# Kernel tuning notes

Measured on AMD Instinct MI355X. Metric: run time of the kernel, lower is better.

Reference implementation:

```python
import jax, jax.numpy as jnp
import numpy as np

B, N, D = 1, 128, 64
H, DH = 8, 64            # heads, per-head dim; dim_inner = dim*dim_head = 512
DI = H * DH              # 512
L = 2                    # max_degree
S = 1 + 2 * L            # 5 degree slots: (h, r_1..L, x_1..L)
MLP = 1024               # int(2.0 * dim_inner)
EPS = 1e-5


def _ln(x, g):
    m = x.mean(-1, keepdims=True)
    v = ((x - m) ** 2).mean(-1, keepdims=True)
    return (x - m) * jax.lax.rsqrt(v + EPS) * g


def setup_inputs() -> dict:
    key = jax.random.key(0)
    ks = jax.random.split(key, 16)
    rn = lambda k, s, sc=1.0: jax.random.normal(k, s, dtype=jnp.float32) * sc
    return {
        "h": rn(ks[0], (B, N, D)),
        "t_ij": rn(ks[1], (B, N, N, D)),
        "r1": rn(ks[2], (B, N, N, 3)),
        "r2": rn(ks[3], (B, N, N, 5)),
        "x1": rn(ks[4], (B, N, D, 3)),
        "x2": rn(ks[5], (B, N, D, 5)),
        "g_hi": jnp.ones((D,), jnp.float32),
        "g_hj": jnp.ones((D,), jnp.float32),
        "Wq": rn(ks[6], (D, DI), D ** -0.5),
        "Wk": rn(ks[7], (D, DI), D ** -0.5),
        "Wv1": rn(ks[8], (D, MLP), D ** -0.5),
        "bv1": jnp.zeros((MLP,), jnp.float32),
        "Wv2": rn(ks[9], (MLP, S * DI), MLP ** -0.5),
        "bv2": jnp.zeros((S * DI,), jnp.float32),
        "Wp1": rn(ks[10], (D, MLP), D ** -0.5),
        "bp1": jnp.zeros((MLP,), jnp.float32),
        "Wp2": rn(ks[11], (MLP, S * DI), MLP ** -0.5),
        "bp2": jnp.zeros((S * DI,), jnp.float32),
        "Wev": rn(ks[12], (D, S * DI), D ** -0.5),
        "Wc": rn(ks[13], (DI, D), DI ** -0.5),
    }


def reference(h, t_ij, r1, r2, x1, x2, g_hi, g_hj, Wq, Wk, Wv1, bv1, Wv2, bv2,
              Wp1, bp1, Wp2, bp2, Wev, Wc):
    b, n, d = h.shape
    hi, hj = _ln(h, g_hi), _ln(h, g_hj)
    q = (hi @ Wq).reshape(b, n, H, DH).transpose(0, 2, 1, 3)                # b h i d
    k = (hj @ Wk).reshape(b, n, H, DH).transpose(0, 2, 1, 3)                # b h j d
    vals = (jax.nn.silu(hj @ Wv1 + bv1) @ Wv2 + bv2)
    vals = vals.reshape(b, n, S, H, DH).transpose(0, 3, 1, 2, 4)            # b h j s d
    pav = (jax.nn.silu(hj @ Wp1 + bp1) @ Wp2 + bp2)
    pav = pav.reshape(b, n, S, H, DH).transpose(0, 3, 1, 2, 4)              # b h j s d
    # NOTE: source uses to_edge_values for BOTH edge keys and edge values (to_edge_keys is dead code)
    ev = (t_ij @ Wev).reshape(b, n, n, S, H, DH).transpose(0, 4, 1, 2, 3, 5)  # b h i j s d
    sim_num = jnp.einsum('bhid,bhjd->bhij', q, k)                           # b h i j
    sim_den = jnp.einsum('bhid,bhijsd->bhis', q, ev)                        # b h i s
    attn = sim_num[..., None] / sim_den[:, :, :, None, :]                   # b h i j s (quotient attention)
    sea = attn[..., None] * vals[:, :, None] + ev * pav[:, :, None]         # b h i j s d
    out = sea.transpose(0, 2, 3, 4, 1, 5).reshape(b, n, n, S, DI) @ Wc      # b i j s D
    # split sizes (1, L, L) along the s axis: h scale, r_ij scales, x scales
    h_new = h + out[:, :, :, 0, :].sum(axis=2)                              # sum over neighbors j
    xs, rs = (x1, x2), (r1, r2)
    x_new = [jnp.einsum('bjdm,bijd->bidm', xs[l], out[:, :, :, 1 + L + l, :])
             + jnp.einsum('bijm,bijd->bidm', rs[l], out[:, :, :, 1 + l, :])
             for l in range(L)]
    return (h_new, x_new[0], x_new[1])
```

## Files before the change

### kernel.cpp

```cpp
#include <hip/hip_runtime.h>
#include <hip/hip_bf16.h>

typedef __hip_bfloat16 bf16;
typedef __attribute__((ext_vector_type(8))) short short8;
typedef __attribute__((ext_vector_type(4))) float f32x4;

#define NN 128
#define DD_ 64
#define HH_ 8
#define DH_ 64
#define DI_ 512
#define SS_ 5
#define MLPD 1024
#define SDI 2560

__device__ __forceinline__ float wave_sum64(float v) {
#pragma unroll
    for (int off = 32; off > 0; off >>= 1) v += __shfl_xor(v, off, 64);
    return v;
}

__device__ __forceinline__ unsigned short f2bf_u(float f) {
    unsigned u = __float_as_uint(f);
    u += 0x7FFF + ((u >> 16) & 1);
    return (unsigned short)(u >> 16);
}
__device__ __forceinline__ float bfu2f(unsigned short s) {
    return __uint_as_float(((unsigned)s) << 16);
}
__device__ __forceinline__ unsigned pk2(unsigned short a, unsigned short b) {
    return (unsigned)a | ((unsigned)b << 16);
}

__global__ __launch_bounds__(256) void k_front(
    const float* __restrict__ h, const float* __restrict__ ghi, const float* __restrict__ ghj,
    const float* __restrict__ Wq, const float* __restrict__ Wk,
    const float* __restrict__ Wv1, const float* __restrict__ bv1,
    const float* __restrict__ Wp1, const float* __restrict__ bp1,
    float* __restrict__ q, float* __restrict__ k,
    float* __restrict__ a1, float* __restrict__ p1) {
    int i = blockIdx.x, ch = blockIdx.y, t = threadIdx.x;
    int d = t & 63;
    __shared__ float hib[DD_], hjb[DD_];
    float x = h[i * DD_ + d];
    float s = wave_sum64(x);
    float s2 = wave_sum64(x * x);
    float m = s * (1.0f / DD_);
    float v = s2 * (1.0f / DD_) - m * m;
    float r = rsqrtf(v + 1e-5f);
    float xc = (x - m) * r;
    if (t < 64) { hib[d] = xc * ghi[d]; hjb[d] = xc * ghj[d]; }
    __syncthreads();
    {
        int c = ch * 128 + (t & 127);
        const float* W = (t < 128) ? Wq : Wk;
        const float* hb = (t < 128) ? hib : hjb;
        float a = 0.f;
#pragma unroll 8
        for (int dd = 0; dd < DD_; dd++) a += hb[dd] * W[dd * DI_ + c];
        float* dstqk = (t < 128) ? q : k;
        dstqk[i * DI_ + c] = a;
    }
    {
        int c = ch * 256 + t;
        float av = 0.f, ap = 0.f;
#pragma unroll 4
        for (int dd = 0; dd < DD_; dd++) {
            float hv = hjb[dd];
            av += hv * Wv1[dd * MLPD + c];
            ap += hv * Wp1[dd * MLPD + c];
        }
        float xv = av + bv1[c], xp = ap + bp1[c];
        a1[i * MLPD + c] = xv / (1.0f + expf(-xv));
        p1[i * MLPD + c] = xp / (1.0f + expf(-xp));
    }
}

#define KS2 4
__global__ __launch_bounds__(256) void k_mlp2(const float* __restrict__ a1,
                                              const float* __restrict__ p1,
                                              const float* __restrict__ Wv2,
                                              const float* __restrict__ Wp2,
                                              float* __restrict__ part) {
    int ct = blockIdx.x, ks = blockIdx.y, t = threadIdx.x;
    int c0 = ct * 64;
    bool isp = c0 >= 2560;
    int c0l = c0 - (isp ? 2560 : 0);
    const float* __restrict__ src = isp ? p1 : a1;
    const float* __restrict__ W = isp ? Wp2 : Wv2;
    int kbase = ks * 256;
    __shared__ unsigned short Ahi[128][40], Alo[128][40];
    __shared__ unsigned short Bhi[64][40], Blo[64][40];
    int lane = t & 63, wv = t >> 6;
    int l15 = lane & 15, quad = lane >> 4;
    f32x4 acc[2][4];
#pragma unroll
    for (int mt = 0; mt < 2; mt++)
#pragma unroll
        for (int nt = 0; nt < 4; nt++) acc[mt][nt] = (f32x4){0.f, 0.f, 0.f, 0.f};
    int aj = t >> 1, ak = (t & 1) * 16;
    int bc = t & 63, bk = (t >> 6) * 8;
    for (int kc = 0; kc < 8; kc++) {
        int k0 = kbase + kc * 32;
        __syncthreads();
        {
            unsigned short h16[16], l16[16];
            const float* ap = &src[(size_t)aj * MLPD + k0 + ak];
#pragma unroll
            for (int e = 0; e < 16; e += 4) {
                float4 v = *(const float4*)(ap + e);
                float vv[4] = {v.x, v.y, v.z, v.w};
#pragma unroll
                for (int z = 0; z < 4; z++) {
                    unsigned short hb = f2bf_u(vv[z]);
                    h16[e + z] = hb;
                    l16[e + z] = f2bf_u(vv[z] - bfu2f(hb));
                }
            }
            *(uint4*)&Ahi[aj][ak] = make_uint4(pk2(h16[0], h16[1]), pk2(h16[2], h16[3]),
                                               pk2(h16[4], h16[5]), pk2(h16[6], h16[7]));
            *(uint4*)&Ahi[aj][ak + 8] = make_uint4(pk2(h16[8], h16[9]), pk2(h16[10], h16[11]),
                                                   pk2(h16[12], h16[13]), pk2(h16[14], h16[15]));
            *(uint4*)&Alo[aj][ak] = make_uint4(pk2(l16[0], l16[1]), pk2(l16[2], l16[3]),
                                               pk2(l16[4], l16[5]), pk2(l16[6], l16[7]));
            *(uint4*)&Alo[aj][ak + 8] = make_uint4(pk2(l16[8], l16[9]), pk2(l16[10], l16[11]),
                                                   pk2(l16[12], l16[13]), pk2(l16[14], l16[15]));
        }
        {
            unsigned short h8[8], l8[8];
#pragma unroll
            for (int e = 0; e < 8; e++) {
                float v = W[(size_t)(k0 + bk + e) * SDI + c0l + bc];
                unsigned short hb = f2bf_u(v);
                h8[e] = hb;
                l8[e] = f2bf_u(v - bfu2f(hb));
            }
            *(uint4*)&Bhi[bc][bk] = make_uint4(pk2(h8[0], h8[1]), pk2(h8[2], h8[3]),
                                               pk2(h8[4], h8[5]), pk2(h8[6], h8[7]));
            *(uint4*)&Blo[bc][bk] = make_uint4(pk2(l8[0], l8[1]), pk2(l8[2], l8[3]),
                                               pk2(l8[4], l8[5]), pk2(l8[6], l8[7]));
        }
        __syncthreads();
        int ko = quad * 8;
        short8 a_h0 = *(const short8*)&Ahi[(wv * 2 + 0) * 16 + l15][ko];
        short8 a_l0 = *(const short8*)&Alo[(wv * 2 + 0) * 16 + l15][ko];
        short8 a_h1 = *(const short8*)&Ahi[(wv * 2 + 1) * 16 + l15][ko];
        short8 a_l1 = *(const short8*)&Alo[(wv * 2 + 1) * 16 + l15][ko];
#pragma unroll
        for (int nt = 0; nt < 4; nt++) {
            short8 b_h = *(const short8*)&Bhi[nt * 16 + l15][ko];
            short8 b_l = *(const short8*)&Blo[nt * 16 + l15][ko];
            acc[0][nt] = __builtin_amdgcn_mfma_f32_16x16x32_bf16(a_h0, b_h, acc[0][nt], 0, 0, 0);
            acc[0][nt] = __builtin_amdgcn_mfma_f32_16x16x32_bf16(a_h0, b_l, acc[0][nt], 0, 0, 0);
            acc[0][nt] = __builtin_amdgcn_mfma_f32_16x16x32_bf16(a_l0, b_h, acc[0][nt], 0, 0, 0);
            acc[1][nt] = __builtin_amdgcn_mfma_f32_16x16x32_bf16(a_h1, b_h, acc[1][nt], 0, 0, 0);
            acc[1][nt] = __builtin_amdgcn_mfma_f32_16x16x32_bf16(a_h1, b_l, acc[1][nt], 0, 0, 0);
            acc[1][nt] = __builtin_amdgcn_mfma_f32_16x16x32_bf16(a_l1, b_h, acc[1][nt], 0, 0, 0);
        }
    }
#pragma unroll
    for (int mt = 0; mt < 2; mt++)
#pragma unroll
        for (int nt = 0; nt < 4; nt++)
#pragma unroll
            for (int r = 0; r < 4; r++) {
                int j = (wv * 2 + mt) * 16 + quad * 4 + r;
                int cc = c0 + nt * 16 + l15;
                part[(size_t)ks * 655360 + (size_t)j * 5120 + cc] = acc[mt][nt][r];
            }
}

__global__ __launch_bounds__(512) void k_post(const float* __restrict__ part,
                                              const float* __restrict__ bv2,
                                              const float* __restrict__ bp2,
                                              const float* __restrict__ Wc,
                                              float* __restrict__ pav,
                                              float* __restrict__ VC) {
    int j = blockIdx.x, y = blockIdx.y, t = threadIdx.x;
    if (y < 5) {
        int s = y;
        __shared__ float vlds[512];
        int e = s * 512 + t;
        float sum = 0.f;
#pragma unroll
        for (int p = 0; p < KS2; p++) sum += part[(size_t)p * 655360 + (size_t)j * 5120 + e];
        vlds[t] = sum + bv2[e];
        __syncthreads();
        int dd = t & 63;
        int hbase = t - dd;
        float acc = 0.f;
#pragma unroll 8
        for (int d2 = 0; d2 < DH_; d2++) acc += vlds[hbase + d2] * Wc[(size_t)(hbase + d2) * DD_ + dd];
        VC[(size_t)(j * SS_ + s) * DI_ + t] = acc;
    } else {
        int s = y - 5;
        int e = 2560 + s * 512 + t;
        float sum = 0.f;
#pragma unroll
        for (int p = 0; p < KS2; p++) sum += part[(size_t)p * 655360 + (size_t)j * 5120 + e];
        pav[(size_t)j * SDI + s * 512 + t] = sum + bp2[s * 512 + t];
    }
}

__global__ __launch_bounds__(640) void k_den(const float* __restrict__ tij,
                                             const float* __restrict__ Wev,
                                             const float* __restrict__ q,
                                             float* __restrict__ rsd) {
    int i = blockIdx.x, half = blockIdx.y, t = threadIdx.x;
    __shared__ float red[10][64];
    __shared__ float Tl[64];
    __shared__ float ql[DI_];
    int c = t & 63, jw = t >> 6;
    float s = 0.f;
    for (int j = jw; j < NN; j += 10) s += tij[(size_t)(i * NN + j) * DD_ + c];
    red[jw][c] = s;
    if (t < DI_) ql[t] = q[i * DI_ + t];
    __syncthreads();
    if (t < 64) {
        float a = 0.f;
#pragma unroll
        for (int r2 = 0; r2 < 10; r2++) a += red[r2][t];
        Tl[t] = a;
    }
    __syncthreads();
#pragma unroll
    for (int kx = 0; kx < 2; kx++) {
        int u = half * 1280 + kx * 640 + t;
        float ev = 0.f;
#pragma unroll 8
        for (int cc = 0; cc < DD_; cc++) ev += Tl[cc] * Wev[(size_t)cc * SDI + u];
        float den = wave_sum64(ev * ql[u & 511]);
        if ((t & 63) == 0) {
            int g = u >> 6;
            int ss = g >> 3, hh = g & 7;
            rsd[i * 40 + hh * SS_ + ss] = 1.0f / den;
        }
    }
}

__global__ __launch_bounds__(512) void k_simnum(const float* __restrict__ q,
                                                const float* __restrict__ k,
                                                float* __restrict__ sn) {
    int i = blockIdx.x, yh = blockIdx.y, t = threadIdx.x;
    int hh = yh * 4 + (t >> 7), j = t & 127;
    __shared__ float qb[256];
    if (t < 256) qb[t] = q[i * DI_ + yh * 256 + t];
    __syncthreads();
    float a = 0.f;
    const float* kr = &k[(size_t)j * DI_ + hh * DH_];
    const float* qr = &qb[(hh - yh * 4) * DH_];
#pragma unroll 8
    for (int d = 0; d < DH_; d++) a += qr[d] * kr[d];
    sn[i * 1024 + hh * NN + j] = a;
}

#define KCM 64
__global__ __launch_bounds__(256) void k_M(const float* __restrict__ pav,
                                           const float* __restrict__ Wev,
                                           const float* __restrict__ Wc,
                                           float* __restrict__ M) {
    int j = blockIdx.x, s = blockIdx.y, t = threadIdx.x;
    int lane = t & 63, w = t >> 6;
    __shared__ float P[DI_];
    __shared__ unsigned short Ahi[64][72], Alo[64][72];
    __shared__ unsigned short Bhi[64][72], Blo[64][72];
    P[t] = pav[j * SDI + s * DI_ + t];
    P[t + 256] = pav[j * SDI + s * DI_ + t + 256];
    f32x4 acc[4];
#pragma unroll
    for (int n = 0; n < 4; n++) acc[n] = (f32x4){0.f, 0.f, 0.f, 0.f};
    __syncthreads();
    for (int u0 = 0; u0 < DI_; u0 += KCM) {
        {
            int c = t >> 2, ug = (t & 3) * 16;
            const float* wevp = &Wev[(size_t)c * SDI + s * DI_ + u0 + ug];
            unsigned short ah[16], al[16];
#pragma unroll
            for (int e = 0; e < 16; e += 4) {
                float4 wv = *(const float4*)(wevp + e);
                float4 pv = *(const float4*)&P[u0 + ug + e];
                float av[4] = {wv.x * pv.x, wv.y * pv.y, wv.z * pv.z, wv.w * pv.w};
#pragma unroll
                for (int z = 0; z < 4; z++) {
                    unsigned short hh2 = f2bf_u(av[z]);
                    ah[e + z] = hh2;
                    al[e + z] = f2bf_u(av[z] - bfu2f(hh2));
                }
            }
            *(uint4*)&Ahi[c][ug] = make_uint4(pk2(ah[0], ah[1]), pk2(ah[2], ah[3]),
                                              pk2(ah[4], ah[5]), pk2(ah[6], ah[7]));
            *(uint4*)&Ahi[c][ug + 8] = make_uint4(pk2(ah[8], ah[9]), pk2(ah[10], ah[11]),
                                                  pk2(ah[12], ah[13]), pk2(ah[14], ah[15]));
            *(uint4*)&Alo[c][ug] = make_uint4(pk2(al[0], al[1]), pk2(al[2], al[3]),
                                              pk2(al[4], al[5]), pk2(al[6], al[7]));
            *(uint4*)&Alo[c][ug + 8] = make_uint4(pk2(al[8], al[9]), pk2(al[10], al[11]),
                                                  pk2(al[12], al[13]), pk2(al[14], al[15]));
        }
        {
            int dd = t & 63, ub = (t >> 6) * 16;
            unsigned short bh[16], bl[16];
#pragma unroll
            for (int e = 0; e < 16; e++) {
                float v = Wc[(size_t)(u0 + ub + e) * DD_ + dd];
                unsigned short hh2 = f2bf_u(v);
                bh[e] = hh2;
                bl[e] = f2bf_u(v - bfu2f(hh2));
            }
            *(uint4*)&Bhi[dd][ub] = make_uint4(pk2(bh[0], bh[1]), pk2(bh[2], bh[3]),
                                               pk2(bh[4], bh[5]), pk2(bh[6], bh[7]));
            *(uint4*)&Bhi[dd][ub + 8] = make_uint4(pk2(bh[8], bh[9]), pk2(bh[10], bh[11]),
                                                   pk2(bh[12], bh[13]), pk2(bh[14], bh[15]));
            *(uint4*)&Blo[dd][ub] = make_uint4(pk2(bl[0], bl[1]), pk2(bl[2], bl[3]),
                                               pk2(bl[4], bl[5]), pk2(bl[6], bl[7]));
            *(uint4*)&Blo[dd][ub + 8] = make_uint4(pk2(bl[8], bl[9]), pk2(bl[10], bl[11]),
                                                   pk2(bl[12], bl[13]), pk2(bl[14], bl[15]));
        }
        __syncthreads();
#pragma unroll
        for (int kk = 0; kk < 2; kk++) {
            int ko = kk * 32 + (lane >> 4) * 8;
            short8 a_h = *(const short8*)&Ahi[w * 16 + (lane & 15)][ko];
            short8 a_l = *(const short8*)&Alo[w * 16 + (lane & 15)][ko];
#pragma unroll
            for (int n = 0; n < 4; n++) {
                short8 b_h = *(const short8*)&Bhi[n * 16 + (lane & 15)][ko];
                short8 b_l = *(const short8*)&Blo[n * 16 + (lane & 15)][ko];
                acc[n] = __builtin_amdgcn_mfma_f32_16x16x32_bf16(a_h, b_h, acc[n], 0, 0, 0);
                acc[n] = __builtin_amdgcn_mfma_f32_16x16x32_bf16(a_h, b_l, acc[n], 0, 0, 0);
                acc[n] = __builtin_amdgcn_mfma_f32_16x16x32_bf16(a_l, b_h, acc[n], 0, 0, 0);
            }
        }
        __syncthreads();
    }
    float* Mp = &M[(size_t)(j * SS_ + s) * 4096];
#pragma unroll
    for (int n = 0; n < 4; n++)
#pragma unroll
        for (int r = 0; r < 4; r++) {
            int c = w * 16 + (lane >> 4) * 4 + r;
            int dd = n * 16 + (lane & 15);
            Mp[c * 64 + dd] = acc[n][r];
        }
}

__global__ __launch_bounds__(256) void k_out(const float* __restrict__ M, const float* __restrict__ VC,
                                             const float* __restrict__ sn, const float* __restrict__ rsd,
                                             const float* __restrict__ tij, float* __restrict__ outb) {
    int j = blockIdx.x, s = blockIdx.y, t = threadIdx.x;
    int lane = t & 63, wv = t >> 6, l15 = lane & 15, quad = lane >> 4;
    __shared__ unsigned short Ahi[128][40], Alo[128][40];
    __shared__ unsigned short Bhi[64][40], Blo[64][40];
    f32x4 acc[2][4];
#pragma unroll
    for (int mt = 0; mt < 2; mt++)
#pragma unroll
        for (int nt = 0; nt < 4; nt++) acc[mt][nt] = (f32x4){0.f, 0.f, 0.f, 0.f};
    {
        int i = t >> 1, hg = (t & 1) * 4;
        unsigned short h4[4], l4[4];
#pragma unroll
        for (int e = 0; e < 4; e++) {
            int hh_ = hg + e;
            float v = sn[i * 1024 + hh_ * NN + j] * rsd[i * 40 + hh_ * SS_ + s];
            unsigned short hb = f2bf_u(v);
            h4[e] = hb;
            l4[e] = f2bf_u(v - bfu2f(hb));
        }
        *(uint2*)&Ahi[i][hg] = make_uint2(pk2(h4[0], h4[1]), pk2(h4[2], h4[3]));
        *(uint2*)&Alo[i][hg] = make_uint2(pk2(l4[0], l4[1]), pk2(l4[2], l4[3]));
#pragma unroll
        for (int r = 0; r < 2; r++) {
            int idx = t + r * 256;
            if (idx < 384) {
                int ii = idx / 3, g = idx % 3;
                *(uint4*)&Ahi[ii][8 + g * 8] = make_uint4(0, 0, 0, 0);
                *(uint4*)&Alo[ii][8 + g * 8] = make_uint4(0, 0, 0, 0);
            }
        }
        if (t < 64) {
            unsigned short h8[8], l8[8];
#pragma unroll
            for (int e = 0; e < 8; e++) {
                float v = VC[(size_t)(j * SS_ + s) * DI_ + e * 64 + t];
                unsigned short hb = f2bf_u(v);
                h8[e] = hb;
                l8[e] = f2bf_u(v - bfu2f(hb));
            }
            *(uint4*)&Bhi[t][0] = make_uint4(pk2(h8[0], h8[1]), pk2(h8[2], h8[3]),
                                             pk2(h8[4], h8[5]), pk2(h8[6], h8[7]));
            *(uint4*)&Blo[t][0] = make_uint4(pk2(l8[0], l8[1]), pk2(l8[2], l8[3]),
                                             pk2(l8[4], l8[5]), pk2(l8[6], l8[7]));
        } else {
            int idx = t - 64;
            int dd2 = idx / 3, g = idx % 3;
            *(uint4*)&Bhi[dd2][8 + g * 8] = make_uint4(0, 0, 0, 0);
            *(uint4*)&Blo[dd2][8 + g * 8] = make_uint4(0, 0, 0, 0);
        }
    }
    __syncthreads();
    {
        int ko = quad * 8;
        short8 a_h0 = *(const short8*)&Ahi[(wv * 2 + 0) * 16 + l15][ko];
        short8 a_l0 = *(const short8*)&Alo[(wv * 2 + 0) * 16 + l15][ko];
        short8 a_h1 = *(const short8*)&Ahi[(wv * 2 + 1) * 16 + l15][ko];
        short8 a_l1 = *(const short8*)&Alo[(wv * 2 + 1) * 16 + l15][ko];
#pragma unroll
        for (int nt = 0; nt < 4; nt++) {
            short8 b_h = *(const short8*)&Bhi[nt * 16 + l15][ko];
            short8 b_l = *(const short8*)&Blo[nt * 16 + l15][ko];
            acc[0][nt] = __builtin_amdgcn_mfma_f32_16x16x32_bf16(a_h0, b_h, acc[0][nt], 0, 0, 0);
            acc[0][nt] = __builtin_amdgcn_mfma_f32_16x16x32_bf16(a_h0, b_l, acc[0][nt], 0, 0, 0);
            acc[0][nt] = __builtin_amdgcn_mfma_f32_16x16x32_bf16(a_l0, b_h, acc[0][nt], 0, 0, 0);
            acc[1][nt] = __builtin_amdgcn_mfma_f32_16x16x32_bf16(a_h1, b_h, acc[1][nt], 0, 0, 0);
            acc[1][nt] = __builtin_amdgcn_mfma_f32_16x16x32_bf16(a_h1, b_l, acc[1][nt], 0, 0, 0);
            acc[1][nt] = __builtin_amdgcn_mfma_f32_16x16x32_bf16(a_l1, b_h, acc[1][nt], 0, 0, 0);
        }
    }
    for (int kc = 0; kc < 2; kc++) {
        __syncthreads();
        {
            int i = t >> 1, chalf = (t & 1) * 16;
            unsigned short h16[16], l16[16];
            const float* tp = &tij[(size_t)(i * NN + j) * DD_ + kc * 32 + chalf];
#pragma unroll
            for (int e = 0; e < 16; e += 4) {
                float4 v = *(const float4*)(tp + e);
                float vv[4] = {v.x, v.y, v.z, v.w};
#pragma unroll
                for (int z = 0; z < 4; z++) {
                    unsigned short hb = f2bf_u(vv[z]);
                    h16[e + z] = hb;
                    l16[e + z] = f2bf_u(vv[z] - bfu2f(hb));
                }
            }
            *(uint4*)&Ahi[i][chalf] = make_uint4(pk2(h16[0], h16[1]), pk2(h16[2], h16[3]),
                                                 pk2(h16[4], h16[5]), pk2(h16[6], h16[7]));
            *(uint4*)&Ahi[i][chalf + 8] = make_uint4(pk2(h16[8], h16[9]), pk2(h16[10], h16[11]),
                                                     pk2(h16[12], h16[13]), pk2(h16[14], h16[15]));
            *(uint4*)&Alo[i][chalf] = make_uint4(pk2(l16[0], l16[1]), pk2(l16[2], l16[3]),
                                                 pk2(l16[4], l16[5]), pk2(l16[6], l16[7]));
            *(uint4*)&Alo[i][chalf + 8] = make_uint4(pk2(l16[8], l16[9]), pk2(l16[10], l16[11]),
                                                     pk2(l16[12], l16[13]), pk2(l16[14], l16[15]));
        }
        {
            int dd2 = t & 63, cg = (t >> 6) * 8;
            unsigned short h8[8], l8[8];
#pragma unroll
            for (int e = 0; e < 8; e++) {
                float v = M[(size_t)(j * SS_ + s) * 4096 + (size_t)(kc * 32 + cg + e) * 64 + dd2];
                unsigned short hb = f2bf_u(v);
                h8[e] = hb;
                l8[e] = f2bf_u(v - bfu2f(hb));
            }
            *(uint4*)&Bhi[dd2][cg] = make_uint4(pk2(h8[0], h8[1]), pk2(h8[2], h8[3]),
                                                pk2(h8[4], h8[5]), pk2(h8[6], h8[7]));
            *(uint4*)&Blo[dd2][cg] = make_uint4(pk2(l8[0], l8[1]), pk2(l8[2], l8[3]),
                                                pk2(l8[4], l8[5]), pk2(l8[6], l8[7]));
        }
        __syncthreads();
        int ko = quad * 8;
        short8 a_h0 = *(const short8*)&Ahi[(wv * 2 + 0) * 16 + l15][ko];
        short8 a_l0 = *(const short8*)&Alo[(wv * 2 + 0) * 16 + l15][ko];
        short8 a_h1 = *(const short8*)&Ahi[(wv * 2 + 1) * 16 + l15][ko];
        short8 a_l1 = *(const short8*)&Alo[(wv * 2 + 1) * 16 + l15][ko];
#pragma unroll
        for (int nt = 0; nt < 4; nt++) {
            short8 b_h = *(const short8*)&Bhi[nt * 16 + l15][ko];
            short8 b_l = *(const short8*)&Blo[nt * 16 + l15][ko];
            acc[0][nt] = __builtin_amdgcn_mfma_f32_16x16x32_bf16(a_h0, b_h, acc[0][nt], 0, 0, 0);
            acc[0][nt] = __builtin_amdgcn_mfma_f32_16x16x32_bf16(a_h0, b_l, acc[0][nt], 0, 0, 0);
            acc[0][nt] = __builtin_amdgcn_mfma_f32_16x16x32_bf16(a_l0, b_h, acc[0][nt], 0, 0, 0);
            acc[1][nt] = __builtin_amdgcn_mfma_f32_16x16x32_bf16(a_h1, b_h, acc[1][nt], 0, 0, 0);
            acc[1][nt] = __builtin_amdgcn_mfma_f32_16x16x32_bf16(a_h1, b_l, acc[1][nt], 0, 0, 0);
            acc[1][nt] = __builtin_amdgcn_mfma_f32_16x16x32_bf16(a_l1, b_h, acc[1][nt], 0, 0, 0);
        }
    }
#pragma unroll
    for (int mt = 0; mt < 2; mt++)
#pragma unroll
        for (int nt = 0; nt < 4; nt++)
#pragma unroll
            for (int r = 0; r < 4; r++) {
                int i = (wv * 2 + mt) * 16 + quad * 4 + r;
                int dd = nt * 16 + l15;
                outb[((size_t)(i * NN + j) * SS_ + s) * 64 + dd] = acc[mt][nt][r];
            }
}

#define JC 16
#define JPC 8
__global__ void k_red1(const float* __restrict__ outb,
                       const float* __restrict__ r1, const float* __restrict__ r2,
                       const float* __restrict__ x1, const float* __restrict__ x2,
                       float* __restrict__ pr) {
    int i = blockIdx.x, jc = blockIdx.y, t = threadIdx.x;
    int s = t >> 6, dd = t & 63;
    int jbeg = jc * JPC;
    float hacc = 0.f;
    float am[5] = {0.f, 0.f, 0.f, 0.f, 0.f};
    for (int jj = 0; jj < JPC; jj++) {
        int j = jbeg + jj;
        float ov = outb[((size_t)(i * NN + j) * SS_ + s) * 64 + dd];
        if (s == 0) {
            hacc += ov;
        } else if (s == 1) {
#pragma unroll
            for (int m = 0; m < 3; m++) am[m] += r1[(i * NN + j) * 3 + m] * ov;
        } else if (s == 2) {
#pragma unroll
            for (int m = 0; m < 5; m++) am[m] += r2[(i * NN + j) * 5 + m] * ov;
        } else if (s == 3) {
#pragma unroll
            for (int m = 0; m < 3; m++) am[m] += x1[(j * DD_ + dd) * 3 + m] * ov;
        } else {
#pragma unroll
            for (int m = 0; m < 5; m++) am[m] += x2[(j * DD_ + dd) * 5 + m] * ov;
        }
    }
    float* rec = &pr[(size_t)(i * JC + jc) * 1088];
    if (s == 0) {
        rec[dd] = hacc;
    } else if (s == 1) {
#pragma unroll
        for (int m = 0; m < 3; m++) rec[64 + dd * 3 + m] = am[m];
    } else if (s == 2) {
#pragma unroll
        for (int m = 0; m < 5; m++) rec[256 + dd * 5 + m] = am[m];
    } else if (s == 3) {
#pragma unroll
        for (int m = 0; m < 3; m++) rec[576 + dd * 3 + m] = am[m];
    } else {
#pragma unroll
        for (int m = 0; m < 5; m++) rec[768 + dd * 5 + m] = am[m];
    }
}

__global__ void k_red2(const float* __restrict__ pr, const float* __restrict__ h,
                       float* __restrict__ dst) {
    int i = blockIdx.x, t = threadIdx.x;
    int s = t >> 6, dd = t & 63;
    const float* base = &pr[(size_t)i * JC * 1088];
    if (s == 0) {
        float v = 0.f;
#pragma unroll
        for (int c = 0; c < JC; c++) v += base[c * 1088 + dd];
        dst[i * DD_ + dd] = h[i * DD_ + dd] + v;
    } else if (s == 3) {
        float v[3] = {0.f, 0.f, 0.f};
#pragma unroll
        for (int c = 0; c < JC; c++) {
#pragma unroll
            for (int m = 0; m < 3; m++)
                v[m] += base[c * 1088 + 64 + dd * 3 + m] + base[c * 1088 + 576 + dd * 3 + m];
        }
#pragma unroll
        for (int m = 0; m < 3; m++)
            dst[8192 + (i * DD_ + dd) * 3 + m] = v[m];
    } else if (s == 4) {
        float v[5] = {0.f, 0.f, 0.f, 0.f, 0.f};
#pragma unroll
        for (int c = 0; c < JC; c++) {
#pragma unroll
            for (int m = 0; m < 5; m++)
                v[m] += base[c * 1088 + 256 + dd * 5 + m] + base[c * 1088 + 768 + dd * 5 + m];
        }
#pragma unroll
        for (int m = 0; m < 5; m++)
            dst[8192 + 24576 + (i * DD_ + dd) * 5 + m] = v[m];
    }
}

extern "C" void kernel_launch(void* const* d_in, const int* in_sizes, int n_in,
                              void* d_out, int out_size, void* d_ws, size_t ws_size,
                              hipStream_t stream) {
    const float* h_in = (const float*)d_in[0];
    const float* tij = (const float*)d_in[1];
    const float* r1 = (const float*)d_in[2];
    const float* r2 = (const float*)d_in[3];
    const float* x1 = (const float*)d_in[4];
    const float* x2 = (const float*)d_in[5];
    const float* ghi = (const float*)d_in[6];
    const float* ghj = (const float*)d_in[7];
    const float* Wq = (const float*)d_in[8];
    const float* Wk = (const float*)d_in[9];
    const float* Wv1 = (const float*)d_in[10];
    const float* bv1 = (const float*)d_in[11];
    const float* Wv2 = (const float*)d_in[12];
    const float* bv2 = (const float*)d_in[13];
    const float* Wp1 = (const float*)d_in[14];
    const float* bp1 = (const float*)d_in[15];
    const float* Wp2 = (const float*)d_in[16];
    const float* bp2 = (const float*)d_in[17];
    const float* Wev = (const float*)d_in[18];
    const float* Wc = (const float*)d_in[19];
    float* dst = (float*)d_out;

    float* w = (float*)d_ws;
    size_t off = 16;
    auto alloc = [&](size_t n) { float* p = w + off; off += n; return p; };
    float* q    = alloc(65536);
    float* k    = alloc(65536);
    float* a1   = alloc(131072);
    float* p1   = alloc(131072);
    float* pav  = alloc(327680);
    float* VC   = alloc(327680);
    float* sn   = alloc(131072);
    float* rsd  = alloc(5120);
    float* M    = alloc(2621440);
    float* outb = alloc(5242880);
    float* part = alloc(2621440);
    float* pr   = alloc(2228224);

    k_front<<<dim3(128, 4), dim3(256), 0, stream>>>(h_in, ghi, ghj, Wq, Wk, Wv1, bv1, Wp1, bp1,
                                                    q, k, a1, p1);
    k_mlp2<<<dim3(80, KS2), dim3(256), 0, stream>>>(a1, p1, Wv2, Wp2, part);
    k_post<<<dim3(128, 10), dim3(512), 0, stream>>>(part, bv2, bp2, Wc, pav, VC);
    k_den<<<dim3(128, 2), dim3(640), 0, stream>>>(tij, Wev, q, rsd);
    k_simnum<<<dim3(128, 2), dim3(512), 0, stream>>>(q, k, sn);
    k_M<<<dim3(128, 5), dim3(256), 0, stream>>>(pav, Wev, Wc, M);
    k_out<<<dim3(128, 5), dim3(256), 0, stream>>>(M, VC, sn, rsd, tij, outb);
    k_red1<<<dim3(128, JC), dim3(320), 0, stream>>>(outb, r1, r2, x1, x2, pr);
    k_red2<<<dim3(128), dim3(320), 0, stream>>>(pr, h_in, dst);
}
```

Baseline: 204.6 us.

## Merge independent mid-stage kernels into combined launches and fuse final reductions

Independent stages (MLP2 GEMM, edge-denominator, sim numerator) now run as one grid partitioned by block index. Post-processing of the values and the M computation (pav folded into the Wev multiply) are merged into a second kernel, so the pav buffer is never written. The two-stage j-reduction becomes a single 640-thread kernel that reduces through LDS. This cuts the launch count from nine to five and removes intermediate round trips to global memory, at the cost of larger heterogeneous kernels with uneven work per block.

```diff
diff --git a/kernel.cpp b/kernel.cpp
--- a/kernel.cpp
+++ b/kernel.cpp
@@ -13,6 +13,8 @@
 #define SS_ 5
 #define MLPD 1024
 #define SDI 2560
+#define KS2 4
+#define KCM 64
 
 __device__ __forceinline__ float wave_sum64(float v) {
 #pragma unroll
@@ -76,71 +78,331 @@
     }
 }
 
-#define KS2 4
-__global__ __launch_bounds__(256) void k_mlp2(const float* __restrict__ a1,
-                                              const float* __restrict__ p1,
-                                              const float* __restrict__ Wv2,
-                                              const float* __restrict__ Wp2,
-                                              float* __restrict__ part) {
-    int ct = blockIdx.x, ks = blockIdx.y, t = threadIdx.x;
-    int c0 = ct * 64;
-    bool isp = c0 >= 2560;
-    int c0l = c0 - (isp ? 2560 : 0);
-    const float* __restrict__ src = isp ? p1 : a1;
-    const float* __restrict__ W = isp ? Wp2 : Wv2;
-    int kbase = ks * 256;
+__global__ __launch_bounds__(256) void k_mid(
+    const float* __restrict__ a1, const float* __restrict__ p1,
+    const float* __restrict__ Wv2, const float* __restrict__ Wp2,
+    float* __restrict__ part,
+    const float* __restrict__ tij, const float* __restrict__ Wev,
+    const float* __restrict__ q, float* __restrict__ rsd,
+    const float* __restrict__ k, float* __restrict__ sn) {
+    __shared__ __align__(16) unsigned char smem[30720];
+    int b = blockIdx.x, t = threadIdx.x;
+    if (b < 320) {
+        unsigned short (*Ahi)[40] = (unsigned short (*)[40])(smem);
+        unsigned short (*Alo)[40] = (unsigned short (*)[40])(smem + 10240);
+        unsigned short (*Bhi)[40] = (unsigned short (*)[40])(smem + 20480);
+        unsigned short (*Blo)[40] = (unsigned short (*)[40])(smem + 25600);
+        int ct = b % 80, ks = b / 80;
+        int c0 = ct * 64;
+        bool isp = c0 >= 2560;
+        int c0l = c0 - (isp ? 2560 : 0);
+        const float* __restrict__ src = isp ? p1 : a1;
+        const float* __restrict__ W = isp ? Wp2 : Wv2;
+        int kbase = ks * 256;
+        int lane = t & 63, wv = t >> 6;
+        int l15 = lane & 15, quad = lane >> 4;
+        f32x4 acc[2][4];
+#pragma unroll
+        for (int mt = 0; mt < 2; mt++)
+#pragma unroll
+            for (int nt = 0; nt < 4; nt++) acc[mt][nt] = (f32x4){0.f, 0.f, 0.f, 0.f};
+        int aj = t >> 1, ak = (t & 1) * 16;
+        int bc = t & 63, bk = (t >> 6) * 8;
+        for (int kc = 0; kc < 8; kc++) {
+            int k0 = kbase + kc * 32;
+            __syncthreads();
+            {
+                unsigned short h16[16], l16[16];
+                const float* ap = &src[(size_t)aj * MLPD + k0 + ak];
+#pragma unroll
+                for (int e = 0; e < 16; e += 4) {
+                    float4 v = *(const float4*)(ap + e);
+                    float vv[4] = {v.x, v.y, v.z, v.w};
+#pragma unroll
+                    for (int z = 0; z < 4; z++) {
+                        unsigned short hb = f2bf_u(vv[z]);
+                        h16[e + z] = hb;
+                        l16[e + z] = f2bf_u(vv[z] - bfu2f(hb));
+                    }
+                }
+                *(uint4*)&Ahi[aj][ak] = make_uint4(pk2(h16[0], h16[1]), pk2(h16[2], h16[3]),
+                                                   pk2(h16[4], h16[5]), pk2(h16[6], h16[7]));
+                *(uint4*)&Ahi[aj][ak + 8] = make_uint4(pk2(h16[8], h16[9]), pk2(h16[10], h16[11]),
+                                                       pk2(h16[12], h16[13]), pk2(h16[14], h16[15]));
+                *(uint4*)&Alo[aj][ak] = make_uint4(pk2(l16[0], l16[1]), pk2(l16[2], l16[3]),
+                                                   pk2(l16[4], l16[5]), pk2(l16[6], l16[7]));
+                *(uint4*)&Alo[aj][ak + 8] = make_uint4(pk2(l16[8], l16[9]), pk2(l16[10], l16[11]),
+                                                       pk2(l16[12], l16[13]), pk2(l16[14], l16[15]));
+            }
+            {
+                unsigned short h8[8], l8[8];
+#pragma unroll
+                for (int e = 0; e < 8; e++) {
+                    float v = W[(size_t)(k0 + bk + e) * SDI + c0l + bc];
+                    unsigned short hb = f2bf_u(v);
+                    h8[e] = hb;
+                    l8[e] = f2bf_u(v - bfu2f(hb));
+                }
+                *(uint4*)&Bhi[bc][bk] = make_uint4(pk2(h8[0], h8[1]), pk2(h8[2], h8[3]),
+                                                   pk2(h8[4], h8[5]), pk2(h8[6], h8[7]));
+                *(uint4*)&Blo[bc][bk] = make_uint4(pk2(l8[0], l8[1]), pk2(l8[2], l8[3]),
+                                                   pk2(l8[4], l8[5]), pk2(l8[6], l8[7]));
+            }
+            __syncthreads();
+            int ko = quad * 8;
+            short8 a_h0 = *(const short8*)&Ahi[(wv * 2 + 0) * 16 + l15][ko];
+            short8 a_l0 = *(const short8*)&Alo[(wv * 2 + 0) * 16 + l15][ko];
+            short8 a_h1 = *(const short8*)&Ahi[(wv * 2 + 1) * 16 + l15][ko];
+            short8 a_l1 = *(const short8*)&Alo[(wv * 2 + 1) * 16 + l15][ko];
+#pragma unroll
+            for (int nt = 0; nt < 4; nt++) {
+                short8 b_h = *(const short8*)&Bhi[nt * 16 + l15][ko];
+                short8 b_l = *(const short8*)&Blo[nt * 16 + l15][ko];
+                acc[0][nt] = __builtin_amdgcn_mfma_f32_16x16x32_bf16(a_h0, b_h, acc[0][nt], 0, 0, 0);
+                acc[0][nt] = __builtin_amdgcn_mfma_f32_16x16x32_bf16(a_h0, b_l, acc[0][nt], 0, 0, 0);
+                acc[0][nt] = __builtin_amdgcn_mfma_f32_16x16x32_bf16(a_l0, b_h, acc[0][nt], 0, 0, 0);
+                acc[1][nt] = __builtin_amdgcn_mfma_f32_16x16x32_bf16(a_h1, b_h, acc[1][nt], 0, 0, 0);
+                acc[1][nt] = __builtin_amdgcn_mfma_f32_16x16x32_bf16(a_h1, b_l, acc[1][nt], 0, 0, 0);
+                acc[1][nt] = __builtin_amdgcn_mfma_f32_16x16x32_bf16(a_l1, b_h, acc[1][nt], 0, 0, 0);
+            }
+        }
+#pragma unroll
+        for (int mt = 0; mt < 2; mt++)
+#pragma unroll
+            for (int nt = 0; nt < 4; nt++)
+#pragma unroll
+                for (int r = 0; r < 4; r++) {
+                    int j = (wv * 2 + mt) * 16 + quad * 4 + r;
+                    int cc = c0 + nt * 16 + l15;
+                    part[(size_t)ks * 655360 + (size_t)j * 5120 + cc] = acc[mt][nt][r];
+                }
+    } else if (b < 448) {
+        float* red = (float*)smem;
+        float* Tl = (float*)(smem + 1024);
+        float* ql = (float*)(smem + 1280);
+        int i = b - 320;
+        int c = t & 63, jw = t >> 6;
+        float s = 0.f;
+        for (int j = jw; j < NN; j += 4) s += tij[(size_t)(i * NN + j) * DD_ + c];
+        red[jw * 64 + c] = s;
+        ql[t] = q[i * DI_ + t];
+        ql[t + 256] = q[i * DI_ + t + 256];
+        __syncthreads();
+        if (t < 64) Tl[t] = red[t] + red[64 + t] + red[128 + t] + red[192 + t];
+        __syncthreads();
+#pragma unroll
+        for (int kx = 0; kx < 10; kx++) {
+            int u = kx * 256 + t;
+            float ev = 0.f;
+#pragma unroll 8
+            for (int cc = 0; cc < DD_; cc++) ev += Tl[cc] * Wev[(size_t)cc * SDI + u];
+            float den = wave_sum64(ev * ql[u & 511]);
+            if ((t & 63) == 0) {
+                int g = u >> 6;
+                int ss = g >> 3, hh = g & 7;
+                rsd[i * 40 + hh * SS_ + ss] = 1.0f / den;
+            }
+        }
+    } else {
+        float* qb = (float*)smem;
+        int idx = b - 448;
+        int i = idx & 127, yh = idx >> 7;
+        if (t < 128) qb[t] = q[i * DI_ + yh * 128 + t];
+        __syncthreads();
+        int hh = yh * 2 + (t >> 7), j = t & 127;
+        float a = 0.f;
+        const float* kr = &k[(size_t)j * DI_ + hh * DH_];
+        const float* qr = &qb[(t >> 7) * 64];
+#pragma unroll 8
+        for (int d = 0; d < DH_; d++) a += qr[d] * kr[d];
+        sn[i * 1024 + hh * NN + j] = a;
+    }
+}
+
+__global__ __launch_bounds__(256) void k_mid2(
+    const float* __restrict__ part, const float* __restrict__ bv2,
+    const float* __restrict__ bp2, const float* __restrict__ Wc,
+    const float* __restrict__ Wev, float* __restrict__ VC, float* __restrict__ M) {
+    __shared__ __align__(16) unsigned char smem[38912];
+    int b = blockIdx.x, t = threadIdx.x;
+    if (b < 640) {
+        float* vlds = (float*)smem;
+        int j = b & 127, s = b >> 7;
+#pragma unroll
+        for (int r = 0; r < 2; r++) {
+            int tt = r * 256 + t;
+            int e = s * 512 + tt;
+            float sum = 0.f;
+#pragma unroll
+            for (int p = 0; p < KS2; p++) sum += part[(size_t)p * 655360 + (size_t)j * 5120 + e];
+            vlds[tt] = sum + bv2[e];
+        }
+        __syncthreads();
+#pragma unroll
+        for (int r = 0; r < 2; r++) {
+            int tt = r * 256 + t;
+            int dd = tt & 63;
+            int hbase = tt - dd;
+            float acc = 0.f;
+#pragma unroll 8
+            for (int d2 = 0; d2 < DH_; d2++)
+                acc += vlds[hbase + d2] * Wc[(size_t)(hbase + d2) * DD_ + dd];
+            VC[(size_t)(j * SS_ + s) * DI_ + tt] = acc;
+        }
+    } else {
+        int idx = b - 640;
+        int j = idx & 127, s = idx >> 7;
+        int lane = t & 63, w = t >> 6;
+        float* P = (float*)smem;
+        unsigned short (*Ahi)[72] = (unsigned short (*)[72])(smem + 2048);
+        unsigned short (*Alo)[72] = (unsigned short (*)[72])(smem + 11264);
+        unsigned short (*Bhi)[72] = (unsigned short (*)[72])(smem + 20480);
+        unsigned short (*Blo)[72] = (unsigned short (*)[72])(smem + 29696);
+        {
+            int e = 2560 + s * 512 + t;
+            float s0 = 0.f, s1 = 0.f;
+#pragma unroll
+            for (int p = 0; p < KS2; p++) {
+                s0 += part[(size_t)p * 655360 + (size_t)j * 5120 + e];
+                s1 += part[(size_t)p * 655360 + (size_t)j * 5120 + e + 256];
+            }
+            P[t] = s0 + bp2[s * 512 + t];
+            P[t + 256] = s1 + bp2[s * 512 + t + 256];
+        }
+        f32x4 acc[4];
+#pragma unroll
+        for (int n = 0; n < 4; n++) acc[n] = (f32x4){0.f, 0.f, 0.f, 0.f};
+        __syncthreads();
+        for (int u0 = 0; u0 < DI_; u0 += KCM) {
+            {
+                int c = t >> 2, ug = (t & 3) * 16;
+                const float* wevp = &Wev[(size_t)c * SDI + s * DI_ + u0 + ug];
+                unsigned short ah[16], al[16];
+#pragma unroll
+                for (int e = 0; e < 16; e += 4) {
+                    float4 wv = *(const float4*)(wevp + e);
+                    float4 pv = *(const float4*)&P[u0 + ug + e];
+                    float av[4] = {wv.x * pv.x, wv.y * pv.y, wv.z * pv.z, wv.w * pv.w};
+#pragma unroll
+                    for (int z = 0; z < 4; z++) {
+                        unsigned short hh2 = f2bf_u(av[z]);
+                        ah[e + z] = hh2;
+                        al[e + z] = f2bf_u(av[z] - bfu2f(hh2));
+                    }
+                }
+                *(uint4*)&Ahi[c][ug] = make_uint4(pk2(ah[0], ah[1]), pk2(ah[2], ah[3]),
+                                                  pk2(ah[4], ah[5]), pk2(ah[6], ah[7]));
+                *(uint4*)&Ahi[c][ug + 8] = make_uint4(pk2(ah[8], ah[9]), pk2(ah[10], ah[11]),
+                                                      pk2(ah[12], ah[13]), pk2(ah[14], ah[15]));
+                *(uint4*)&Alo[c][ug] = make_uint4(pk2(al[0], al[1]), pk2(al[2], al[3]),
+                                                  pk2(al[4], al[5]), pk2(al[6], al[7]));
+                *(uint4*)&Alo[c][ug + 8] = make_uint4(pk2(al[8], al[9]), pk2(al[10], al[11]),
+                                                      pk2(al[12], al[13]), pk2(al[14], al[15]));
+            }
+            {
+                int dd = t & 63, ub = (t >> 6) * 16;
+                unsigned short bh[16], bl[16];
+#pragma unroll
+                for (int e = 0; e < 16; e++) {
+                    float v = Wc[(size_t)(u0 + ub + e) * DD_ + dd];
+                    unsigned short hh2 = f2bf_u(v);
+                    bh[e] = hh2;
+                    bl[e] = f2bf_u(v - bfu2f(hh2));
+                }
+                *(uint4*)&Bhi[dd][ub] = make_uint4(pk2(bh[0], bh[1]), pk2(bh[2], bh[3]),
+                                                   pk2(bh[4], bh[5]), pk2(bh[6], bh[7]));
+                *(uint4*)&Bhi[dd][ub + 8] = make_uint4(pk2(bh[8], bh[9]), pk2(bh[10], bh[11]),
+                                                       pk2(bh[12], bh[13]), pk2(bh[14], bh[15]));
+                *(uint4*)&Blo[dd][ub] = make_uint4(pk2(bl[0], bl[1]), pk2(bl[2], bl[3]),
+                                                   pk2(bl[4], bl[5]), pk2(bl[6], bl[7]));
+                *(uint4*)&Blo[dd][ub + 8] = make_uint4(pk2(bl[8], bl[9]), pk2(bl[10], bl[11]),
+                                                       pk2(bl[12], bl[13]), pk2(bl[14], bl[15]));
+            }
+            __syncthreads();
+#pragma unroll
+            for (int kk = 0; kk < 2; kk++) {
+                int ko = kk * 32 + (lane >> 4) * 8;
+                short8 a_h = *(const short8*)&Ahi[w * 16 + (lane & 15)][ko];
+                short8 a_l = *(const short8*)&Alo[w * 16 + (lane & 15)][ko];
+#pragma unroll
+                for (int n = 0; n < 4; n++) {
+                    short8 b_h = *(const short8*)&Bhi[n * 16 + (lane & 15)][ko];
+                    short8 b_l = *(const short8*)&Blo[n * 16 + (lane & 15)][ko];
+                    acc[n] = __builtin_amdgcn_mfma_f32_16x16x32_bf16(a_h, b_h, acc[n], 0, 0, 0);
+                    acc[n] = __builtin_amdgcn_mfma_f32_16x16x32_bf16(a_h, b_l, acc[n], 0, 0, 0);
+                    acc[n] = __builtin_amdgcn_mfma_f32_16x16x32_bf16(a_l, b_h, acc[n], 0, 0, 0);
+                }
+            }
+            __syncthreads();
+        }
+        float* Mp = &M[(size_t)(j * SS_ + s) * 4096];
+#pragma unroll
+        for (int n = 0; n < 4; n++)
+#pragma unroll
+            for (int r = 0; r < 4; r++) {
+                int c = w * 16 + (lane >> 4) * 4 + r;
+                int dd = n * 16 + (lane & 15);
+                Mp[c * 64 + dd] = acc[n][r];
+            }
+    }
+}
+
+__global__ __launch_bounds__(256) void k_out(const float* __restrict__ M, const float* __restrict__ VC,
+                                             const float* __restrict__ sn, const float* __restrict__ rsd,
+                                             const float* __restrict__ tij, float* __restrict__ outb) {
+    int j = blockIdx.x, s = blockIdx.y, t = threadIdx.x;
+    int lane = t & 63, wv = t >> 6, l15 = lane & 15, quad = lane >> 4;
     __shared__ unsigned short Ahi[128][40], Alo[128][40];
     __shared__ unsigned short Bhi[64][40], Blo[64][40];
-    int lane = t & 63, wv = t >> 6;
-    int l15 = lane & 15, quad = lane >> 4;
     f32x4 acc[2][4];
 #pragma unroll
     for (int mt = 0; mt < 2; mt++)
 #pragma unroll
         for (int nt = 0; nt < 4; nt++) acc[mt][nt] = (f32x4){0.f, 0.f, 0.f, 0.f};
-    int aj = t >> 1, ak = (t & 1) * 16;
-    int bc = t & 63, bk = (t >> 6) * 8;
-    for (int kc = 0; kc < 8; kc++) {
-        int k0 = kbase + kc * 32;
-        __syncthreads();
-        {
-            unsigned short h16[16], l16[16];
-            const float* ap = &src[(size_t)aj * MLPD + k0 + ak];
-#pragma unroll
-            for (int e = 0; e < 16; e += 4) {
-                float4 v = *(const float4*)(ap + e);
-                float vv[4] = {v.x, v.y, v.z, v.w};
-#pragma unroll
-                for (int z = 0; z < 4; z++) {
-                    unsigned short hb = f2bf_u(vv[z]);
-                    h16[e + z] = hb;
-                    l16[e + z] = f2bf_u(vv[z] - bfu2f(hb));
-                }
-            }
-            *(uint4*)&Ahi[aj][ak] = make_uint4(pk2(h16[0], h16[1]), pk2(h16[2], h16[3]),
-                                               pk2(h16[4], h16[5]), pk2(h16[6], h16[7]));
-            *(uint4*)&Ahi[aj][ak + 8] = make_uint4(pk2(h16[8], h16[9]), pk2(h16[10], h16[11]),
-                                                   pk2(h16[12], h16[13]), pk2(h16[14], h16[15]));
-            *(uint4*)&Alo[aj][ak] = make_uint4(pk2(l16[0], l16[1]), pk2(l16[2], l16[3]),
-                                               pk2(l16[4], l16[5]), pk2(l16[6], l16[7]));
-            *(uint4*)&Alo[aj][ak + 8] = make_uint4(pk2(l16[8], l16[9]), pk2(l16[10], l16[11]),
-                                                   pk2(l16[12], l16[13]), pk2(l16[14], l16[15]));
-        }
-        {
+    {
+        int i = t >> 1, hg = (t & 1) * 4;
+        unsigned short h4[4], l4[4];
+#pragma unroll
+        for (int e = 0; e < 4; e++) {
+            int hh_ = hg + e;
+            float v = sn[i * 1024 + hh_ * NN + j] * rsd[i * 40 + hh_ * SS_ + s];
+            unsigned short hb = f2bf_u(v);
+            h4[e] = hb;
+            l4[e] = f2bf_u(v - bfu2f(hb));
+        }
+        *(uint2*)&Ahi[i][hg] = make_uint2(pk2(h4[0], h4[1]), pk2(h4[2], h4[3]));
+        *(uint2*)&Alo[i][hg] = make_uint2(pk2(l4[0], l4[1]), pk2(l4[2], l4[3]));
+#pragma unroll
+        for (int r = 0; r < 2; r++) {
+            int idx = t + r * 256;
+            if (idx < 384) {
+                int ii = idx / 3, g = idx % 3;
+                *(uint4*)&Ahi[ii][8 + g * 8] = make_uint4(0, 0, 0, 0);
+                *(uint4*)&Alo[ii][8 + g * 8] = make_uint4(0, 0, 0, 0);
+            }
+        }
+        if (t < 64) {
             unsigned short h8[8], l8[8];
 #pragma unroll
             for (int e = 0; e < 8; e++) {
-                float v = W[(size_t)(k0 + bk + e) * SDI + c0l + bc];
+                float v = VC[(size_t)(j * SS_ + s) * DI_ + e * 64 + t];
                 unsigned short hb = f2bf_u(v);
                 h8[e] = hb;
                 l8[e] = f2bf_u(v - bfu2f(hb));
             }
-            *(uint4*)&Bhi[bc][bk] = make_uint4(pk2(h8[0], h8[1]), pk2(h8[2], h8[3]),
-                                               pk2(h8[4], h8[5]), pk2(h8[6], h8[7]));
-            *(uint4*)&Blo[bc][bk] = make_uint4(pk2(l8[0], l8[1]), pk2(l8[2], l8[3]),
-                                               pk2(l8[4], l8[5]), pk2(l8[6], l8[7]));
-        }
-        __syncthreads();
+            *(uint4*)&Bhi[t][0] = make_uint4(pk2(h8[0], h8[1]), pk2(h8[2], h8[3]),
+                                             pk2(h8[4], h8[5]), pk2(h8[6], h8[7]));
+            *(uint4*)&Blo[t][0] = make_uint4(pk2(l8[0], l8[1]), pk2(l8[2], l8[3]),
+                                             pk2(l8[4], l8[5]), pk2(l8[6], l8[7]));
+        } else {
+            int idx = t - 64;
+            int dd2 = idx / 3, g = idx % 3;
+            *(uint4*)&Bhi[dd2][8 + g * 8] = make_uint4(0, 0, 0, 0);
+            *(uint4*)&Blo[dd2][8 + g * 8] = make_uint4(0, 0, 0, 0);
+        }
+    }
+    __syncthreads();
+    {
         int ko = quad * 8;
         short8 a_h0 = *(const short8*)&Ahi[(wv * 2 + 0) * 16 + l15][ko];
         short8 a_l0 = *(const short8*)&Alo[(wv * 2 + 0) * 16 + l15][ko];
@@ -158,247 +420,48 @@
             acc[1][nt] = __builtin_amdgcn_mfma_f32_16x16x32_bf16(a_l1, b_h, acc[1][nt], 0, 0, 0);
         }
     }
-#pragma unroll
-    for (int mt = 0; mt < 2; mt++)
-#pragma unroll
-        for (int nt = 0; nt < 4; nt++)
-#pragma unroll
-            for (int r = 0; r < 4; r++) {
-                int j = (wv * 2 + mt) * 16 + quad * 4 + r;
-                int cc = c0 + nt * 16 + l15;
-                part[(size_t)ks * 655360 + (size_t)j * 5120 + cc] = acc[mt][nt][r];
-            }
-}
-
-__global__ __launch_bounds__(512) void k_post(const float* __restrict__ part,
-                                              const float* __restrict__ bv2,
-                                              const float* __restrict__ bp2,
-                                              const float* __restrict__ Wc,
-                                              float* __restrict__ pav,
-                                              float* __restrict__ VC) {
-    int j = blockIdx.x, y = blockIdx.y, t = threadIdx.x;
-    if (y < 5) {
-        int s = y;
-        __shared__ float vlds[512];
-        int e = s * 512 + t;
-        float sum = 0.f;
-#pragma unroll
-        for (int p = 0; p < KS2; p++) sum += part[(size_t)p * 655360 + (size_t)j * 5120 + e];
-        vlds[t] = sum + bv2[e];
-        __syncthreads();
-        int dd = t & 63;
-        int hbase = t - dd;
-        float acc = 0.f;
-#pragma unroll 8
-        for (int d2 = 0; d2 < DH_; d2++) acc += vlds[hbase + d2] * Wc[(size_t)(hbase + d2) * DD_ + dd];
-        VC[(size_t)(j * SS_ + s) * DI_ + t] = acc;
-    } else {
-        int s = y - 5;
-        int e = 2560 + s * 512 + t;
-        float sum = 0.f;
-#pragma unroll
-        for (int p = 0; p < KS2; p++) sum += part[(size_t)p * 655360 + (size_t)j * 5120 + e];
-        pav[(size_t)j * SDI + s * 512 + t] = sum + bp2[s * 512 + t];
-    }
-}
-
-__global__ __launch_bounds__(640) void k_den(const float* __restrict__ tij,
-                                             const float* __restrict__ Wev,
-                                             const float* __restrict__ q,
-                                             float* __restrict__ rsd) {
-    int i = blockIdx.x, half = blockIdx.y, t = threadIdx.x;
-    __shared__ float red[10][64];
-    __shared__ float Tl[64];
-    __shared__ float ql[DI_];
-    int c = t & 63, jw = t >> 6;
-    float s = 0.f;
-    for (int j = jw; j < NN; j += 10) s += tij[(size_t)(i * NN + j) * DD_ + c];
-    red[jw][c] = s;
-    if (t < DI_) ql[t] = q[i * DI_ + t];
-    __syncthreads();
-    if (t < 64) {
-        float a = 0.f;
-#pragma unroll
-        for (int r2 = 0; r2 < 10; r2++) a += red[r2][t];
-        Tl[t] = a;
-    }
-    __syncthreads();
-#pragma unroll
-    for (int kx = 0; kx < 2; kx++) {
-        int u = half * 1280 + kx * 640 + t;
-        float ev = 0.f;
-#pragma unroll 8
-        for (int cc = 0; cc < DD_; cc++) ev += Tl[cc] * Wev[(size_t)cc * SDI + u];
-        float den = wave_sum64(ev * ql[u & 511]);
-        if ((t & 63) == 0) {
-            int g = u >> 6;
-            int ss = g >> 3, hh = g & 7;
-            rsd[i * 40 + hh * SS_ + ss] = 1.0f / den;
-        }
-    }
-}
-
-__global__ __launch_bounds__(512) void k_simnum(const float* __restrict__ q,
-                                                const float* __restrict__ k,
-                                                float* __restrict__ sn) {
-    int i = blockIdx.x, yh = blockIdx.y, t = threadIdx.x;
-    int hh = yh * 4 + (t >> 7), j = t & 127;
-    __shared__ float qb[256];
-    if (t < 256) qb[t] = q[i * DI_ + yh * 256 + t];
-    __syncthreads();
-    float a = 0.f;
-    const float* kr = &k[(size_t)j * DI_ + hh * DH_];
-    const float* qr = &qb[(hh - yh * 4) * DH_];
-#pragma unroll 8
-    for (int d = 0; d < DH_; d++) a += qr[d] * kr[d];
-    sn[i * 1024 + hh * NN + j] = a;
-}
-
-#define KCM 64
-__global__ __launch_bounds__(256) void k_M(const float* __restrict__ pav,
-                                           const float* __restrict__ Wev,
-                                           const float* __restrict__ Wc,
-                                           float* __restrict__ M) {
-    int j = blockIdx.x, s = blockIdx.y, t = threadIdx.x;
-    int lane = t & 63, w = t >> 6;
-    __shared__ float P[DI_];
-    __shared__ unsigned short Ahi[64][72], Alo[64][72];
-    __shared__ unsigned short Bhi[64][72], Blo[64][72];
-    P[t] = pav[j * SDI + s * DI_ + t];
-    P[t + 256] = pav[j * SDI + s * DI_ + t + 256];
-    f32x4 acc[4];
-#pragma unroll
-    for (int n = 0; n < 4; n++) acc[n] = (f32x4){0.f, 0.f, 0.f, 0.f};
-    __syncthreads();
-    for (int u0 = 0; u0 < DI_; u0 += KCM) {
+    for (int kc = 0; kc < 2; kc++) {
+        __syncthreads();
         {
-            int c = t >> 2, ug = (t & 3) * 16;
-            const float* wevp = &Wev[(size_t)c * SDI + s * DI_ + u0 + ug];
-            unsigned short ah[16], al[16];
+            int i = t >> 1, chalf = (t & 1) * 16;
+            unsigned short h16[16], l16[16];
+            const float* tp = &tij[(size_t)(i * NN + j) * DD_ + kc * 32 + chalf];
 #pragma unroll
             for (int e = 0; e < 16; e += 4) {
-                float4 wv = *(const float4*)(wevp + e);
-                float4 pv = *(const float4*)&P[u0 + ug + e];
-                float av[4] = {wv.x * pv.x, wv.y * pv.y, wv.z * pv.z, wv.w * pv.w};
+                float4 v = *(const float4*)(tp + e);
+                float vv[4] = {v.x, v.y, v.z, v.w};
 #pragma unroll
                 for (int z = 0; z < 4; z++) {
-                    unsigned short hh2 = f2bf_u(av[z]);
-                    ah[e + z] = hh2;
-                    al[e + z] = f2bf_u(av[z] - bfu2f(hh2));
-                }
-            }
-            *(uint4*)&Ahi[c][ug] = make_uint4(pk2(ah[0], ah[1]), pk2(ah[2], ah[3]),
-                                              pk2(ah[4], ah[5]), pk2(ah[6], ah[7]));
-            *(uint4*)&Ahi[c][ug + 8] = make_uint4(pk2(ah[8], ah[9]), pk2(ah[10], ah[11]),
-                                                  pk2(ah[12], ah[13]), pk2(ah[14], ah[15]));
-            *(uint4*)&Alo[c][ug] = make_uint4(pk2(al[0], al[1]), pk2(al[2], al[3]),
-                                              pk2(al[4], al[5]), pk2(al[6], al[7]));
-            *(uint4*)&Alo[c][ug + 8] = make_uint4(pk2(al[8], al[9]), pk2(al[10], al[11]),
-                                                  pk2(al[12], al[13]), pk2(al[14], al[15]));
+                    unsigned short hb = f2bf_u(vv[z]);
+                    h16[e + z] = hb;
+                    l16[e + z] = f2bf_u(vv[z] - bfu2f(hb));
+                }
+            }
+            *(uint4*)&Ahi[i][chalf] = make_uint4(pk2(h16[0], h16[1]), pk2(h16[2], h16[3]),
+                                                 pk2(h16[4], h16[5]), pk2(h16[6], h16[7]));
+            *(uint4*)&Ahi[i][chalf + 8] = make_uint4(pk2(h16[8], h16[9]), pk2(h16[10], h16[11]),
+                                                     pk2(h16[12], h16[13]), pk2(h16[14], h16[15]));
+            *(uint4*)&Alo[i][chalf] = make_uint4(pk2(l16[0], l16[1]), pk2(l16[2], l16[3]),
+                                                 pk2(l16[4], l16[5]), pk2(l16[6], l16[7]));
+            *(uint4*)&Alo[i][chalf + 8] = make_uint4(pk2(l16[8], l16[9]), pk2(l16[10], l16[11]),
+                                                     pk2(l16[12], l16[13]), pk2(l16[14], l16[15]));
         }
         {
-            int dd = t & 63, ub = (t >> 6) * 16;
-            unsigned short bh[16], bl[16];
-#pragma unroll
-            for (int e = 0; e < 16; e++) {
-                float v = Wc[(size_t)(u0 + ub + e) * DD_ + dd];
-                unsigned short hh2 = f2bf_u(v);
-                bh[e] = hh2;
-                bl[e] = f2bf_u(v - bfu2f(hh2));
-            }
-            *(uint4*)&Bhi[dd][ub] = make_uint4(pk2(bh[0], bh[1]), pk2(bh[2], bh[3]),
-                                               pk2(bh[4], bh[5]), pk2(bh[6], bh[7]));
-            *(uint4*)&Bhi[dd][ub + 8] = make_uint4(pk2(bh[8], bh[9]), pk2(bh[10], bh[11]),
-                                                   pk2(bh[12], bh[13]), pk2(bh[14], bh[15]));
-            *(uint4*)&Blo[dd][ub] = make_uint4(pk2(bl[0], bl[1]), pk2(bl[2], bl[3]),
-                                               pk2(bl[4], bl[5]), pk2(bl[6], bl[7]));
-            *(uint4*)&Blo[dd][ub + 8] = make_uint4(pk2(bl[8], bl[9]), pk2(bl[10], bl[11]),
-                                                   pk2(bl[12], bl[13]), pk2(bl[14], bl[15]));
-        }
-        __syncthreads();
-#pragma unroll
-        for (int kk = 0; kk < 2; kk++) {
-            int ko = kk * 32 + (lane >> 4) * 8;
-            short8 a_h = *(const short8*)&Ahi[w * 16 + (lane & 15)][ko];
-            short8 a_l = *(const short8*)&Alo[w * 16 + (lane & 15)][ko];
-#pragma unroll
-            for (int n = 0; n < 4; n++) {
-                short8 b_h = *(const short8*)&Bhi[n * 16 + (lane & 15)][ko];
-                short8 b_l = *(const short8*)&Blo[n * 16 + (lane & 15)][ko];
-                acc[n] = __builtin_amdgcn_mfma_f32_16x16x32_bf16(a_h, b_h, acc[n], 0, 0, 0);
-                acc[n] = __builtin_amdgcn_mfma_f32_16x16x32_bf16(a_h, b_l, acc[n], 0, 0, 0);
-                acc[n] = __builtin_amdgcn_mfma_f32_16x16x32_bf16(a_l, b_h, acc[n], 0, 0, 0);
-            }
-        }
-        __syncthreads();
-    }
-    float* Mp = &M[(size_t)(j * SS_ + s) * 4096];
-#pragma unroll
-    for (int n = 0; n < 4; n++)
-#pragma unroll
-        for (int r = 0; r < 4; r++) {
-            int c = w * 16 + (lane >> 4) * 4 + r;
-            int dd = n * 16 + (lane & 15);
-            Mp[c * 64 + dd] = acc[n][r];
-        }
-}
-
-__global__ __launch_bounds__(256) void k_out(const float* __restrict__ M, const float* __restrict__ VC,
-                                             const float* __restrict__ sn, const float* __restrict__ rsd,
-                                             const float* __restrict__ tij, float* __restrict__ outb) {
-    int j = blockIdx.x, s = blockIdx.y, t = threadIdx.x;
-    int lane = t & 63, wv = t >> 6, l15 = lane & 15, quad = lane >> 4;
-    __shared__ unsigned short Ahi[128][40], Alo[128][40];
-    __shared__ unsigned short Bhi[64][40], Blo[64][40];
-    f32x4 acc[2][4];
-#pragma unroll
-    for (int mt = 0; mt < 2; mt++)
-#pragma unroll
-        for (int nt = 0; nt < 4; nt++) acc[mt][nt] = (f32x4){0.f, 0.f, 0.f, 0.f};
-    {
-        int i = t >> 1, hg = (t & 1) * 4;
-        unsigned short h4[4], l4[4];
-#pragma unroll
-        for (int e = 0; e < 4; e++) {
-            int hh_ = hg + e;
-            float v = sn[i * 1024 + hh_ * NN + j] * rsd[i * 40 + hh_ * SS_ + s];
-            unsigned short hb = f2bf_u(v);
-            h4[e] = hb;
-            l4[e] = f2bf_u(v - bfu2f(hb));
-        }
-        *(uint2*)&Ahi[i][hg] = make_uint2(pk2(h4[0], h4[1]), pk2(h4[2], h4[3]));
-        *(uint2*)&Alo[i][hg] = make_uint2(pk2(l4[0], l4[1]), pk2(l4[2], l4[3]));
-#pragma unroll
-        for (int r = 0; r < 2; r++) {
-            int idx = t + r * 256;
-            if (idx < 384) {
-                int ii = idx / 3, g = idx % 3;
-                *(uint4*)&Ahi[ii][8 + g * 8] = make_uint4(0, 0, 0, 0);
-                *(uint4*)&Alo[ii][8 + g * 8] = make_uint4(0, 0, 0, 0);
-            }
-        }
-        if (t < 64) {
+            int dd2 = t & 63, cg = (t >> 6) * 8;
             unsigned short h8[8], l8[8];
 #pragma unroll
             for (int e = 0; e < 8; e++) {
-                float v = VC[(size_t)(j * SS_ + s) * DI_ + e * 64 + t];
+                float v = M[(size_t)(j * SS_ + s) * 4096 + (size_t)(kc * 32 + cg + e) * 64 + dd2];
                 unsigned short hb = f2bf_u(v);
                 h8[e] = hb;
                 l8[e] = f2bf_u(v - bfu2f(hb));
             }
-            *(uint4*)&Bhi[t][0] = make_uint4(pk2(h8[0], h8[1]), pk2(h8[2], h8[3]),
-                                             pk2(h8[4], h8[5]), pk2(h8[6], h8[7]));
-            *(uint4*)&Blo[t][0] = make_uint4(pk2(l8[0], l8[1]), pk2(l8[2], l8[3]),
-                                             pk2(l8[4], l8[5]), pk2(l8[6], l8[7]));
-        } else {
-            int idx = t - 64;
-            int dd2 = idx / 3, g = idx % 3;
-            *(uint4*)&Bhi[dd2][8 + g * 8] = make_uint4(0, 0, 0, 0);
-            *(uint4*)&Blo[dd2][8 + g * 8] = make_uint4(0, 0, 0, 0);
-        }
-    }
-    __syncthreads();
-    {
+            *(uint4*)&Bhi[dd2][cg] = make_uint4(pk2(h8[0], h8[1]), pk2(h8[2], h8[3]),
+                                                pk2(h8[4], h8[5]), pk2(h8[6], h8[7]));
+            *(uint4*)&Blo[dd2][cg] = make_uint4(pk2(l8[0], l8[1]), pk2(l8[2], l8[3]),
+                                                pk2(l8[4], l8[5]), pk2(l8[6], l8[7]));
+        }
+        __syncthreads();
         int ko = quad * 8;
         short8 a_h0 = *(const short8*)&Ahi[(wv * 2 + 0) * 16 + l15][ko];
         short8 a_l0 = *(const short8*)&Alo[(wv * 2 + 0) * 16 + l15][ko];
@@ -416,65 +479,6 @@
             acc[1][nt] = __builtin_amdgcn_mfma_f32_16x16x32_bf16(a_l1, b_h, acc[1][nt], 0, 0, 0);
         }
     }
-    for (int kc = 0; kc < 2; kc++) {
-        __syncthreads();
-        {
-            int i = t >> 1, chalf = (t & 1) * 16;
-            unsigned short h16[16], l16[16];
-            const float* tp = &tij[(size_t)(i * NN + j) * DD_ + kc * 32 + chalf];
-#pragma unroll
-            for (int e = 0; e < 16; e += 4) {
-                float4 v = *(const float4*)(tp + e);
-                float vv[4] = {v.x, v.y, v.z, v.w};
-#pragma unroll
-                for (int z = 0; z < 4; z++) {
-                    unsigned short hb = f2bf_u(vv[z]);
-                    h16[e + z] = hb;
-                    l16[e + z] = f2bf_u(vv[z] - bfu2f(hb));
-                }
-            }
-            *(uint4*)&Ahi[i][chalf] = make_uint4(pk2(h16[0], h16[1]), pk2(h16[2], h16[3]),
-                                                 pk2(h16[4], h16[5]), pk2(h16[6], h16[7]));
-            *(uint4*)&Ahi[i][chalf + 8] = make_uint4(pk2(h16[8], h16[9]), pk2(h16[10], h16[11]),
-                                                     pk2(h16[12], h16[13]), pk2(h16[14], h16[15]));
-            *(uint4*)&Alo[i][chalf] = make_uint4(pk2(l16[0], l16[1]), pk2(l16[2], l16[3]),
-                                                 pk2(l16[4], l16[5]), pk2(l16[6], l16[7]));
-            *(uint4*)&Alo[i][chalf + 8] = make_uint4(pk2(l16[8], l16[9]), pk2(l16[10], l16[11]),
-                                                     pk2(l16[12], l16[13]), pk2(l16[14], l16[15]));
-        }
-        {
-            int dd2 = t & 63, cg = (t >> 6) * 8;
-            unsigned short h8[8], l8[8];
-#pragma unroll
-            for (int e = 0; e < 8; e++) {
-                float v = M[(size_t)(j * SS_ + s) * 4096 + (size_t)(kc * 32 + cg + e) * 64 + dd2];
-                unsigned short hb = f2bf_u(v);
-                h8[e] = hb;
-                l8[e] = f2bf_u(v - bfu2f(hb));
-            }
-            *(uint4*)&Bhi[dd2][cg] = make_uint4(pk2(h8[0], h8[1]), pk2(h8[2], h8[3]),
-                                                pk2(h8[4], h8[5]), pk2(h8[6], h8[7]));
-            *(uint4*)&Blo[dd2][cg] = make_uint4(pk2(l8[0], l8[1]), pk2(l8[2], l8[3]),
-                                                pk2(l8[4], l8[5]), pk2(l8[6], l8[7]));
-        }
-        __syncthreads();
-        int ko = quad * 8;
-        short8 a_h0 = *(const short8*)&Ahi[(wv * 2 + 0) * 16 + l15][ko];
-        short8 a_l0 = *(const short8*)&Alo[(wv * 2 + 0) * 16 + l15][ko];
-        short8 a_h1 = *(const short8*)&Ahi[(wv * 2 + 1) * 16 + l15][ko];
-        short8 a_l1 = *(const short8*)&Alo[(wv * 2 + 1) * 16 + l15][ko];
-#pragma unroll
-        for (int nt = 0; nt < 4; nt++) {
-            short8 b_h = *(const short8*)&Bhi[nt * 16 + l15][ko];
-            short8 b_l = *(const short8*)&Blo[nt * 16 + l15][ko];
-            acc[0][nt] = __builtin_amdgcn_mfma_f32_16x16x32_bf16(a_h0, b_h, acc[0][nt], 0, 0, 0);
-            acc[0][nt] = __builtin_amdgcn_mfma_f32_16x16x32_bf16(a_h0, b_l, acc[0][nt], 0, 0, 0);
-            acc[0][nt] = __builtin_amdgcn_mfma_f32_16x16x32_bf16(a_l0, b_h, acc[0][nt], 0, 0, 0);
-            acc[1][nt] = __builtin_amdgcn_mfma_f32_16x16x32_bf16(a_h1, b_h, acc[1][nt], 0, 0, 0);
-            acc[1][nt] = __builtin_amdgcn_mfma_f32_16x16x32_bf16(a_h1, b_l, acc[1][nt], 0, 0, 0);
-            acc[1][nt] = __builtin_amdgcn_mfma_f32_16x16x32_bf16(a_l1, b_h, acc[1][nt], 0, 0, 0);
-        }
-    }
 #pragma unroll
     for (int mt = 0; mt < 2; mt++)
 #pragma unroll
@@ -487,22 +491,21 @@
             }
 }
 
-#define JC 16
-#define JPC 8
-__global__ void k_red1(const float* __restrict__ outb,
-                       const float* __restrict__ r1, const float* __restrict__ r2,
-                       const float* __restrict__ x1, const float* __restrict__ x2,
-                       float* __restrict__ pr) {
-    int i = blockIdx.x, jc = blockIdx.y, t = threadIdx.x;
-    int s = t >> 6, dd = t & 63;
-    int jbeg = jc * JPC;
-    float hacc = 0.f;
+__global__ __launch_bounds__(640) void k_redF(const float* __restrict__ outb,
+                                              const float* __restrict__ r1, const float* __restrict__ r2,
+                                              const float* __restrict__ x1, const float* __restrict__ x2,
+                                              const float* __restrict__ h, float* __restrict__ dst) {
+    int i = blockIdx.x, t = threadIdx.x;
+    int half = (t >= 320) ? 1 : 0;
+    int tt = t - half * 320;
+    int s = tt >> 6, dd = tt & 63;
     float am[5] = {0.f, 0.f, 0.f, 0.f, 0.f};
-    for (int jj = 0; jj < JPC; jj++) {
+    int jbeg = half * 64;
+    for (int jj = 0; jj < 64; jj++) {
         int j = jbeg + jj;
         float ov = outb[((size_t)(i * NN + j) * SS_ + s) * 64 + dd];
         if (s == 0) {
-            hacc += ov;
+            am[0] += ov;
         } else if (s == 1) {
 #pragma unroll
             for (int m = 0; m < 3; m++) am[m] += r1[(i * NN + j) * 3 + m] * ov;
@@ -517,56 +520,27 @@
             for (int m = 0; m < 5; m++) am[m] += x2[(j * DD_ + dd) * 5 + m] * ov;
         }
     }
-    float* rec = &pr[(size_t)(i * JC + jc) * 1088];
-    if (s == 0) {
-        rec[dd] = hacc;
-    } else if (s == 1) {
-#pragma unroll
-        for (int m = 0; m < 3; m++) rec[64 + dd * 3 + m] = am[m];
-    } else if (s == 2) {
-#pragma unroll
-        for (int m = 0; m < 5; m++) rec[256 + dd * 5 + m] = am[m];
-    } else if (s == 3) {
-#pragma unroll
-        for (int m = 0; m < 3; m++) rec[576 + dd * 3 + m] = am[m];
-    } else {
-#pragma unroll
-        for (int m = 0; m < 5; m++) rec[768 + dd * 5 + m] = am[m];
-    }
-}
-
-__global__ void k_red2(const float* __restrict__ pr, const float* __restrict__ h,
-                       float* __restrict__ dst) {
-    int i = blockIdx.x, t = threadIdx.x;
-    int s = t >> 6, dd = t & 63;
-    const float* base = &pr[(size_t)i * JC * 1088];
-    if (s == 0) {
-        float v = 0.f;
-#pragma unroll
-        for (int c = 0; c < JC; c++) v += base[c * 1088 + dd];
-        dst[i * DD_ + dd] = h[i * DD_ + dd] + v;
-    } else if (s == 3) {
-        float v[3] = {0.f, 0.f, 0.f};
-#pragma unroll
-        for (int c = 0; c < JC; c++) {
-#pragma unroll
-            for (int m = 0; m < 3; m++)
-                v[m] += base[c * 1088 + 64 + dd * 3 + m] + base[c * 1088 + 576 + dd * 3 + m];
-        }
-#pragma unroll
-        for (int m = 0; m < 3; m++)
-            dst[8192 + (i * DD_ + dd) * 3 + m] = v[m];
-    } else if (s == 4) {
-        float v[5] = {0.f, 0.f, 0.f, 0.f, 0.f};
-#pragma unroll
-        for (int c = 0; c < JC; c++) {
-#pragma unroll
-            for (int m = 0; m < 5; m++)
-                v[m] += base[c * 1088 + 256 + dd * 5 + m] + base[c * 1088 + 768 + dd * 5 + m];
-        }
-#pragma unroll
-        for (int m = 0; m < 5; m++)
-            dst[8192 + 24576 + (i * DD_ + dd) * 5 + m] = v[m];
+    __shared__ float lds[2][5][64][5];
+#pragma unroll
+    for (int m = 0; m < 5; m++) lds[half][s][dd][m] = am[m];
+    __syncthreads();
+    if (half == 0) {
+        if (s == 0) {
+            float v = lds[0][0][dd][0] + lds[1][0][dd][0];
+            dst[i * DD_ + dd] = h[i * DD_ + dd] + v;
+        } else if (s == 1) {
+#pragma unroll
+            for (int m = 0; m < 3; m++) {
+                float v = lds[0][1][dd][m] + lds[1][1][dd][m] + lds[0][3][dd][m] + lds[1][3][dd][m];
+                dst[8192 + (i * DD_ + dd) * 3 + m] = v;
+            }
+        } else if (s == 2) {
+#pragma unroll
+            for (int m = 0; m < 5; m++) {
+                float v = lds[0][2][dd][m] + lds[1][2][dd][m] + lds[0][4][dd][m] + lds[1][4][dd][m];
+                dst[8192 + 24576 + (i * DD_ + dd) * 5 + m] = v;
+            }
+        }
     }
 }
 
@@ -602,23 +576,17 @@
     float* k    = alloc(65536);
     float* a1   = alloc(131072);
     float* p1   = alloc(131072);
-    float* pav  = alloc(327680);
     float* VC   = alloc(327680);
     float* sn   = alloc(131072);
     float* rsd  = alloc(5120);
     float* M    = alloc(2621440);
     float* outb = alloc(5242880);
     float* part = alloc(2621440);
-    float* pr   = alloc(2228224);
 
     k_front<<<dim3(128, 4), dim3(256), 0, stream>>>(h_in, ghi, ghj, Wq, Wk, Wv1, bv1, Wp1, bp1,
                                                     q, k, a1, p1);
-    k_mlp2<<<dim3(80, KS2), dim3(256), 0, stream>>>(a1, p1, Wv2, Wp2, part);
-    k_post<<<dim3(128, 10), dim3(512), 0, stream>>>(part, bv2, bp2, Wc, pav, VC);
-    k_den<<<dim3(128, 2), dim3(640), 0, stream>>>(tij, Wev, q, rsd);
-    k_simnum<<<dim3(128, 2), dim3(512), 0, stream>>>(q, k, sn);
-    k_M<<<dim3(128, 5), dim3(256), 0, stream>>>(pav, Wev, Wc, M);
+    k_mid<<<dim3(960), dim3(256), 0, stream>>>(a1, p1, Wv2, Wp2, part, tij, Wev, q, rsd, k, sn);
+    k_mid2<<<dim3(1280), dim3(256), 0, stream>>>(part, bv2, bp2, Wc, Wev, VC, M);
     k_out<<<dim3(128, 5), dim3(256), 0, stream>>>(M, VC, sn, rsd, tij, outb);
-    k_red1<<<dim3(128, JC), dim3(320), 0, stream>>>(outb, r1, r2, x1, x2, pr);
-    k_red2<<<dim3(128), dim3(320), 0, stream>>>(pr, h_in, dst);
-}
+    k_redF<<<dim3(128), dim3(640), 0, stream>>>(outb, r1, r2, x1, x2, h_in, dst);
+}
```

Result: slower. 238.1 us (+16.4%).
